# Performance work log

Hardware: AMD Instinct MI355X
Metric: run time of the kernel (lower is better)

The kernel has to match this reference:

```python
import jax, jax.numpy as jnp
import numpy as np

N = 4096
IN_DIM = 512
NUM_HEADS = 8
SUB_DIM = 64
ETA = 0.5
LAMBDA_SPARSE = 0.1
EDGE_PROB = 0.01


def setup_inputs() -> dict:
    key = jax.random.key(0)
    k_h, k_u, k_a = jax.random.split(key, 3)
    H = jax.random.normal(k_h, (N, IN_DIM), dtype=jnp.float32)
    # Per-head orthonormal subspace bases (QR init, as in the torch module)
    raw = jax.random.normal(k_u, (NUM_HEADS, IN_DIM, SUB_DIM), dtype=jnp.float32)
    U = jax.vmap(lambda a: jnp.linalg.qr(a)[0])(raw)  # [K, in_dim, r]
    # Binary adjacency mask with self-loops (float 0/1)
    adj = (jax.random.uniform(k_a, (N, N)) < EDGE_PROB).astype(jnp.float32)
    adj_mask = jnp.maximum(adj, jnp.eye(N, dtype=jnp.float32))
    threshold = jnp.full((IN_DIM,), LAMBDA_SPARSE, dtype=jnp.float32)
    return {"H": H, "adj_mask": adj_mask, "U": U, "threshold": threshold}


def reference(H, adj_mask, U, threshold):
    r = U.shape[-1]
    scale = jnp.asarray(r, H.dtype) ** 0.5
    # Z_k = U_k^T H^T  -> [K, r, n]
    Z = jnp.einsum('kdr,nd->krn', U, H)
    # scores[k, i, j] = Z_k[:, i] . Z_k[:, j] / sqrt(r), masked to neighbors
    scores = jnp.einsum('kri,krj->kij', Z, Z) / scale
    scores = scores + (1.0 - adj_mask) * (-1e9)
    alpha = jax.nn.softmax(scores, axis=-1)          # [K, n, n]
    # Z_agg[k, :, i] = sum_j alpha[k, i, j] * Z_k[:, j]
    Z_agg = jnp.einsum('krj,kij->kri', Z, alpha)      # [K, r, n]
    # project back and sum heads: [n, d]
    agg = jnp.einsum('kdr,kri->id', U, Z_agg)
    H_half = H + ETA * agg
    H_out = jax.nn.relu(H_half - threshold[None, :])
    # orthogonality loss: sum_{k<l} ||U_k^T U_l||_F^2
    gram = jnp.einsum('kdr,lds->klrs', U, U)
    sq = jnp.sum(gram ** 2, axis=(-1, -2))            # [K, K]
    orth_loss = 0.5 * (jnp.sum(sq) - jnp.trace(sq))
    return H_out, orth_loss
```

## Files before the change

kernel.cpp:

```cpp
#include <hip/hip_runtime.h>
#include <hip/hip_bf16.h>

#define NN   4096
#define DD   512
#define KH   8
#define RR   64
#define CAP  128

typedef unsigned short u16;
typedef unsigned int   u32;
typedef __attribute__((ext_vector_type(8))) short short8;
typedef __attribute__((ext_vector_type(4))) float f32x4;

__device__ __forceinline__ float bflo(u32 v){ union{u32 i; float f;} c; c.i = v << 16;        return c.f; }
__device__ __forceinline__ float bfhi(u32 v){ union{u32 i; float f;} c; c.i = v & 0xFFFF0000u; return c.f; }
__device__ __forceinline__ u16 f2bf(float f){ __hip_bfloat16 h = __float2bfloat16(f); return *reinterpret_cast<u16*>(&h); }

__global__ __launch_bounds__(256) void prep_scan(const float* __restrict__ H, const float* __restrict__ U,
                                                 const float* __restrict__ adj,
                                                 u16* __restrict__ Hb, u16* __restrict__ Bt1,
                                                 u16* __restrict__ Bt2,
                                                 int* __restrict__ nlist, int* __restrict__ cnt,
                                                 float* __restrict__ lossP) {
    union SH {
        struct { float tile[64][65]; int list[CAP]; int cntS; } p;
        struct { float UkT[64][20]; float UlT[64][68]; } o;
    };
    __shared__ SH sh;
    __shared__ float red4[4];
    const int b = blockIdx.x, t = threadIdx.x;
    if (b < 4096) {
        const int i = b;
        if (t == 0) sh.p.cntS = 0;
        __syncthreads();
        const float* arow = adj + (size_t)i * NN;
        #pragma unroll
        for (int qq = 0; qq < 4; qq++) {
            int j = (qq * 256 + t) * 4;
            float4 mv = *(const float4*)(arow + j);
            if (mv.x != 0.f) { int p = atomicAdd(&sh.p.cntS, 1); if (p < CAP) sh.p.list[p] = j;     }
            if (mv.y != 0.f) { int p = atomicAdd(&sh.p.cntS, 1); if (p < CAP) sh.p.list[p] = j + 1; }
            if (mv.z != 0.f) { int p = atomicAdd(&sh.p.cntS, 1); if (p < CAP) sh.p.list[p] = j + 2; }
            if (mv.w != 0.f) { int p = atomicAdd(&sh.p.cntS, 1); if (p < CAP) sh.p.list[p] = j + 3; }
        }
        __syncthreads();
        const int n = min(sh.p.cntS, CAP);
        if (t < n) nlist[(size_t)i * CAP + t] = sh.p.list[t];
        if (t == 0) cnt[i] = n;
        return;
    }
    if (b < 6144) {
        size_t id = (size_t)(b - 4096) * 256 + t;
        float4 v = *(const float4*)(H + id * 4);
        ushort4 o; o.x = f2bf(v.x); o.y = f2bf(v.y); o.z = f2bf(v.z); o.w = f2bf(v.w);
        *(ushort4*)(Hb + id * 4) = o;
        return;
    }
    if (b < 6208) {
        const int b2 = b - 6144;
        const int k = b2 >> 3, d0 = (b2 & 7) * 64;
        #pragma unroll
        for (int s = 0; s < 4; s++) {
            int u = t + 256 * s;
            int dd = u >> 4, rq = u & 15;
            float4 v = *(const float4*)(U + ((size_t)(k * DD + d0 + dd)) * RR + rq * 4);
            sh.p.tile[dd][rq * 4 + 0] = v.x; sh.p.tile[dd][rq * 4 + 1] = v.y;
            sh.p.tile[dd][rq * 4 + 2] = v.z; sh.p.tile[dd][rq * 4 + 3] = v.w;
        }
        __syncthreads();
        {   int r = t >> 2;
            #pragma unroll
            for (int ii = 0; ii < 16; ii++) {
                int dd = (t & 3) * 16 + ii;
                Bt1[(size_t)(k * RR + r) * DD + d0 + dd] = f2bf(sh.p.tile[dd][r]);
            }
        }
        {   int dd = t >> 2, rb = (t & 3) * 16;
            #pragma unroll
            for (int ii = 0; ii < 16; ii++) {
                Bt2[(size_t)(d0 + dd) * DD + k * RR + rb + ii] = f2bf(sh.p.tile[dd][rb + ii]);
            }
        }
        return;
    }
    const int ob = b - 6208;
    const int pb = ob >> 2, strip = ob & 3;
    int idx = pb, k = 0, lh = 1;
    #pragma unroll
    for (int kk = 0; kk < 8; kk++) {
        int c = 7 - kk;
        if (idx < c) { k = kk; lh = kk + 1 + idx; break; }
        idx -= c;
    }
    const int r = t & 15;
    const int s0 = (t >> 4) * 4;
    const int r0g = strip * 16;
    const float* Uk = U + (size_t)k  * DD * RR;
    const float* Ul = U + (size_t)lh * DD * RR;
    float a0 = 0.f, a1 = 0.f, a2 = 0.f, a3 = 0.f;
    for (int dc = 0; dc < DD; dc += 64) {
        {   int dd = t >> 2, rq = t & 3;
            *(float4*)&sh.o.UkT[dd][rq * 4] = *(const float4*)(Uk + (size_t)(dc + dd) * RR + r0g + rq * 4);
        }
        #pragma unroll
        for (int s = 0; s < 4; s++) {
            int u = t + 256 * s;
            int dd = u >> 4, sq = u & 15;
            *(float4*)&sh.o.UlT[dd][sq * 4] = *(const float4*)(Ul + (size_t)(dc + dd) * RR + sq * 4);
        }
        __syncthreads();
        #pragma unroll 4
        for (int dd = 0; dd < 64; dd++) {
            float a = sh.o.UkT[dd][r];
            float4 bv = *(const float4*)&sh.o.UlT[dd][s0];
            a0 += a * bv.x; a1 += a * bv.y; a2 += a * bv.z; a3 += a * bv.w;
        }
        __syncthreads();
    }
    float v = a0 * a0 + a1 * a1 + a2 * a2 + a3 * a3;
    #pragma unroll
    for (int off = 32; off; off >>= 1) v += __shfl_down(v, off, 64);
    if ((t & 63) == 0) red4[t >> 6] = v;
    __syncthreads();
    if (t == 0) lossP[ob] = red4[0] + red4[1] + red4[2] + red4[3];
}

__global__ __launch_bounds__(256) void zgemm_mfma(const u16* __restrict__ Hb, const u16* __restrict__ Bt1,
                                                  u16* __restrict__ Zb) {
    __shared__ short As[64][72];
    __shared__ short Bs[64][72];
    const int t = threadIdx.x;
    const int i0 = blockIdx.x * 64, n0 = blockIdx.y * 64;
    const int w = t >> 6, lane = t & 63;
    const int lm = lane & 15, lg = lane >> 4;
    f32x4 acc[4] = {};
    for (int kc = 0; kc < DD; kc += 64) {
        #pragma unroll
        for (int s = 0; s < 2; s++) {
            int c = t + 256 * s; int row = c >> 3, g = c & 7;
            *(short8*)&As[row][g * 8] = *(const short8*)(Hb  + (size_t)(i0 + row) * DD + kc + g * 8);
            *(short8*)&Bs[row][g * 8] = *(const short8*)(Bt1 + (size_t)(n0 + row) * DD + kc + g * 8);
        }
        __syncthreads();
        #pragma unroll
        for (int ks = 0; ks < 64; ks += 32) {
            short8 af = *(const short8*)&As[w * 16 + lm][ks + lg * 8];
            #pragma unroll
            for (int b = 0; b < 4; b++) {
                short8 bfr = *(const short8*)&Bs[b * 16 + lm][ks + lg * 8];
                acc[b] = __builtin_amdgcn_mfma_f32_16x16x32_bf16(af, bfr, acc[b], 0, 0, 0);
            }
        }
        __syncthreads();
    }
    #pragma unroll
    for (int b = 0; b < 4; b++)
        #pragma unroll
        for (int q = 0; q < 4; q++) {
            int row = i0 + w * 16 + lg * 4 + q;
            int col = n0 + b * 16 + lm;
            Zb[(size_t)row * DD + col] = f2bf(acc[b][q]);
        }
}

__global__ __launch_bounds__(512) void attn11(const u16* __restrict__ Zb, const int* __restrict__ nlist,
                                              const int* __restrict__ cnt, u16* __restrict__ Zaggb) {
    const int i = blockIdx.x, t = threadIdx.x;
    const int w = t >> 6, lane = t & 63;
    __shared__ int   nbrS[CAP];
    __shared__ float red[KH][DD];
    __shared__ float lS[KH][KH + 1];
    const int ci = cnt[i];
    if (t < CAP) nbrS[t] = nlist[(size_t)i * CAP + min(t, ci - 1)];
    __syncthreads();

    float a[8];
    {
        uint4 av = *(const uint4*)(Zb + (size_t)i * DD + lane * 8);
        a[0] = bflo(av.x); a[1] = bfhi(av.x); a[2] = bflo(av.y); a[3] = bfhi(av.y);
        a[4] = bflo(av.z); a[5] = bfhi(av.z); a[6] = bflo(av.w); a[7] = bfhi(av.w);
    }

    float l = 0.f;
    float acc[8] = {};
    const int nIt = (ci + 7) >> 3;

    uint4 b0 = *(const uint4*)(Zb + (size_t)nbrS[w] * DD + lane * 8);
    uint4 b1 = *(const uint4*)(Zb + (size_t)nbrS[min(w + 8, CAP - 1)] * DD + lane * 8);

    #define PROCESS(c, val)                                                        \
    {   float zf[8];                                                               \
        zf[0] = bflo(c.x); zf[1] = bfhi(c.x); zf[2] = bflo(c.y); zf[3] = bfhi(c.y);\
        zf[4] = bflo(c.z); zf[5] = bfhi(c.z); zf[6] = bflo(c.w); zf[7] = bfhi(c.w);\
        float s = zf[0]*a[0] + zf[1]*a[1] + zf[2]*a[2] + zf[3]*a[3]                \
                + zf[4]*a[4] + zf[5]*a[5] + zf[6]*a[6] + zf[7]*a[7];               \
        s += __shfl_xor(s, 1); s += __shfl_xor(s, 2); s += __shfl_xor(s, 4);       \
        const float e = (val) ? __expf(s * 0.125f) : 0.f;                          \
        l += e;                                                                    \
        _Pragma("unroll")                                                          \
        for (int d = 0; d < 8; d++) acc[d] += e * zf[d];                           \
    }

    for (int tt = 0; tt < nIt; tt += 2) {
        {
            const uint4 c = b0;
            const int pf = min(w + 8 * (tt + 2), CAP - 1);
            b0 = *(const uint4*)(Zb + (size_t)nbrS[pf] * DD + lane * 8);
            const bool val = (w + 8 * tt) < ci;
            PROCESS(c, val);
        }
        if (tt + 1 < nIt) {
            const uint4 c = b1;
            const int pf = min(w + 8 * (tt + 3), CAP - 1);
            b1 = *(const uint4*)(Zb + (size_t)nbrS[pf] * DD + lane * 8);
            const bool val = (w + 8 * (tt + 1)) < ci;
            PROCESS(c, val);
        }
    }
    #undef PROCESS

    *(float4*)&red[w][lane * 8]     = make_float4(acc[0], acc[1], acc[2], acc[3]);
    *(float4*)&red[w][lane * 8 + 4] = make_float4(acc[4], acc[5], acc[6], acc[7]);
    if ((lane & 7) == 0) lS[w][lane >> 3] = l;
    __syncthreads();

    const int d = t, k = d >> 6;
    float ls = 0.f, sum = 0.f;
    #pragma unroll
    for (int ww = 0; ww < KH; ww++) { ls += lS[ww][k]; sum += red[ww][d]; }
    Zaggb[(size_t)i * DD + d] = f2bf(sum / ls);
}

__global__ __launch_bounds__(256) void outgemm_mfma(const u16* __restrict__ Ab, const u16* __restrict__ Btb,
                                                    const float* __restrict__ H, const float* __restrict__ thr,
                                                    const float* __restrict__ lossP,
                                                    float* __restrict__ out) {
    __shared__ short As[64][72];
    __shared__ short Bs[64][72];
    const int t = threadIdx.x;
    const int i0 = blockIdx.x * 64, n0 = blockIdx.y * 64;
    if (i0 == 0 && n0 == 0 && t < 64) {
        float v = lossP[t] + ((t + 64 < 112) ? lossP[t + 64] : 0.f);
        #pragma unroll
        for (int off = 32; off; off >>= 1) v += __shfl_down(v, off, 64);
        if (t == 0) out[(size_t)NN * DD] = v;
    }
    const int w = t >> 6, lane = t & 63;
    const int lm = lane & 15, lg = lane >> 4;
    f32x4 acc[4] = {};
    for (int kc = 0; kc < DD; kc += 64) {
        #pragma unroll
        for (int s = 0; s < 2; s++) {
            int c = t + 256 * s; int row = c >> 3, g = c & 7;
            *(short8*)&As[row][g * 8] = *(const short8*)(Ab  + (size_t)(i0 + row) * DD + kc + g * 8);
            *(short8*)&Bs[row][g * 8] = *(const short8*)(Btb + (size_t)(n0 + row) * DD + kc + g * 8);
        }
        __syncthreads();
        #pragma unroll
        for (int ks = 0; ks < 64; ks += 32) {
            short8 af = *(const short8*)&As[w * 16 + lm][ks + lg * 8];
            #pragma unroll
            for (int b = 0; b < 4; b++) {
                short8 bfr = *(const short8*)&Bs[b * 16 + lm][ks + lg * 8];
                acc[b] = __builtin_amdgcn_mfma_f32_16x16x32_bf16(af, bfr, acc[b], 0, 0, 0);
            }
        }
        __syncthreads();
    }
    #pragma unroll
    for (int b = 0; b < 4; b++) {
        const int col = n0 + b * 16 + lm;
        const float th = thr[col];
        #pragma unroll
        for (int q = 0; q < 4; q++) {
            int row = i0 + w * 16 + lg * 4 + q;
            float h = H[(size_t)row * DD + col];
            out[(size_t)row * DD + col] = fmaxf(h + 0.5f * acc[b][q] - th, 0.f);
        }
    }
}

extern "C" void kernel_launch(void* const* d_in, const int* in_sizes, int n_in,
                              void* d_out, int out_size, void* d_ws, size_t ws_size,
                              hipStream_t stream) {
    const float* H   = (const float*)d_in[0];
    const float* adj = (const float*)d_in[1];
    const float* U   = (const float*)d_in[2];
    const float* thr = (const float*)d_in[3];
    float* out = (float*)d_out;

    char* ws = (char*)d_ws;
    float* lossP = (float*)ws;
    u16*   Hb    = (u16*)(ws + 1024);
    u16*   Zb    = (u16*)(ws + 1024 + 4u * 1024 * 1024);
    u16*   Zaggb = (u16*)(ws + 1024 + 8u * 1024 * 1024);
    u16*   Bt1   = (u16*)(ws + 1024 + 12u * 1024 * 1024);
    u16*   Bt2   = (u16*)(ws + 1024 + 12u * 1024 * 1024 + 512u * 1024);
    int*   nlist = (int*)(ws + 1024 + 13u * 1024 * 1024);
    int*   cnt   = (int*)(ws + 1024 + 15u * 1024 * 1024 + 512u * 1024);

    prep_scan<<<6320, 256, 0, stream>>>(H, U, adj, Hb, Bt1, Bt2, nlist, cnt, lossP);
    zgemm_mfma<<<dim3(64, 8), 256, 0, stream>>>(Hb, Bt1, Zb);
    attn11<<<NN, 512, 0, stream>>>(Zb, nlist, cnt, Zaggb);
    outgemm_mfma<<<dim3(64, 8), 256, 0, stream>>>(Zaggb, Bt2, H, thr, lossP, out);
}
```

Measured before the change: 173.6 us.

## Use wave-ballot compaction for adjacency scan and reorder prep blocks

The adjacency scan now gives each wavefront one row and compacts neighbor indices with ballot/popcount prefix sums, instead of one block per row using shared-memory atomics. This removes the atomic contention and the block-level syncs, and makes each thread issue 16 independent float4 loads. The slow orthogonality-loss blocks move to the front of the grid and use smaller d-chunks, so that long-latency work starts first. Neighbor order is now deterministic. The larger unrolled load set raises register pressure.

```diff
diff --git a/kernel.cpp b/kernel.cpp
--- a/kernel.cpp
+++ b/kernel.cpp
@@ -9,6 +9,7 @@
 
 typedef unsigned short u16;
 typedef unsigned int   u32;
+typedef unsigned long long u64;
 typedef __attribute__((ext_vector_type(8))) short short8;
 typedef __attribute__((ext_vector_type(4))) float f32x4;
 
@@ -23,106 +24,119 @@
                                                  int* __restrict__ nlist, int* __restrict__ cnt,
                                                  float* __restrict__ lossP) {
     union SH {
-        struct { float tile[64][65]; int list[CAP]; int cntS; } p;
-        struct { float UkT[64][20]; float UlT[64][68]; } o;
+        float tile[64][65];
+        struct { float UkT[32][20]; float UlT[32][68]; } o;
     };
     __shared__ SH sh;
     __shared__ float red4[4];
     const int b = blockIdx.x, t = threadIdx.x;
-    if (b < 4096) {
-        const int i = b;
-        if (t == 0) sh.p.cntS = 0;
-        __syncthreads();
-        const float* arow = adj + (size_t)i * NN;
-        #pragma unroll
-        for (int qq = 0; qq < 4; qq++) {
-            int j = (qq * 256 + t) * 4;
-            float4 mv = *(const float4*)(arow + j);
-            if (mv.x != 0.f) { int p = atomicAdd(&sh.p.cntS, 1); if (p < CAP) sh.p.list[p] = j;     }
-            if (mv.y != 0.f) { int p = atomicAdd(&sh.p.cntS, 1); if (p < CAP) sh.p.list[p] = j + 1; }
-            if (mv.z != 0.f) { int p = atomicAdd(&sh.p.cntS, 1); if (p < CAP) sh.p.list[p] = j + 2; }
-            if (mv.w != 0.f) { int p = atomicAdd(&sh.p.cntS, 1); if (p < CAP) sh.p.list[p] = j + 3; }
-        }
-        __syncthreads();
-        const int n = min(sh.p.cntS, CAP);
-        if (t < n) nlist[(size_t)i * CAP + t] = sh.p.list[t];
-        if (t == 0) cnt[i] = n;
+
+    if (b < 112) {
+        const int ob = b;
+        const int pb = ob >> 2, strip = ob & 3;
+        int idx = pb, k = 0, lh = 1;
+        #pragma unroll
+        for (int kk = 0; kk < 8; kk++) {
+            int c = 7 - kk;
+            if (idx < c) { k = kk; lh = kk + 1 + idx; break; }
+            idx -= c;
+        }
+        const int r = t & 15;
+        const int s0 = (t >> 4) * 4;
+        const int r0g = strip * 16;
+        const float* Uk = U + (size_t)k  * DD * RR;
+        const float* Ul = U + (size_t)lh * DD * RR;
+        float a0 = 0.f, a1 = 0.f, a2 = 0.f, a3 = 0.f;
+        for (int dc = 0; dc < DD; dc += 32) {
+            if (t < 128) {
+                int dd = t >> 2, rq = t & 3;
+                *(float4*)&sh.o.UkT[dd][rq * 4] = *(const float4*)(Uk + (size_t)(dc + dd) * RR + r0g + rq * 4);
+            }
+            #pragma unroll
+            for (int s = 0; s < 2; s++) {
+                int u = t + 256 * s;
+                int dd = u >> 4, sq = u & 15;
+                *(float4*)&sh.o.UlT[dd][sq * 4] = *(const float4*)(Ul + (size_t)(dc + dd) * RR + sq * 4);
+            }
+            __syncthreads();
+            #pragma unroll 4
+            for (int dd = 0; dd < 32; dd++) {
+                float a = sh.o.UkT[dd][r];
+                float4 bv = *(const float4*)&sh.o.UlT[dd][s0];
+                a0 += a * bv.x; a1 += a * bv.y; a2 += a * bv.z; a3 += a * bv.w;
+            }
+            __syncthreads();
+        }
+        float v = a0 * a0 + a1 * a1 + a2 * a2 + a3 * a3;
+        #pragma unroll
+        for (int off = 32; off; off >>= 1) v += __shfl_down(v, off, 64);
+        if ((t & 63) == 0) red4[t >> 6] = v;
+        __syncthreads();
+        if (t == 0) lossP[ob] = red4[0] + red4[1] + red4[2] + red4[3];
         return;
     }
-    if (b < 6144) {
-        size_t id = (size_t)(b - 4096) * 256 + t;
-        float4 v = *(const float4*)(H + id * 4);
-        ushort4 o; o.x = f2bf(v.x); o.y = f2bf(v.y); o.z = f2bf(v.z); o.w = f2bf(v.w);
-        *(ushort4*)(Hb + id * 4) = o;
-        return;
-    }
-    if (b < 6208) {
-        const int b2 = b - 6144;
+    if (b < 176) {
+        const int b2 = b - 112;
         const int k = b2 >> 3, d0 = (b2 & 7) * 64;
         #pragma unroll
         for (int s = 0; s < 4; s++) {
             int u = t + 256 * s;
             int dd = u >> 4, rq = u & 15;
             float4 v = *(const float4*)(U + ((size_t)(k * DD + d0 + dd)) * RR + rq * 4);
-            sh.p.tile[dd][rq * 4 + 0] = v.x; sh.p.tile[dd][rq * 4 + 1] = v.y;
-            sh.p.tile[dd][rq * 4 + 2] = v.z; sh.p.tile[dd][rq * 4 + 3] = v.w;
+            sh.tile[dd][rq * 4 + 0] = v.x; sh.tile[dd][rq * 4 + 1] = v.y;
+            sh.tile[dd][rq * 4 + 2] = v.z; sh.tile[dd][rq * 4 + 3] = v.w;
         }
         __syncthreads();
         {   int r = t >> 2;
             #pragma unroll
             for (int ii = 0; ii < 16; ii++) {
                 int dd = (t & 3) * 16 + ii;
-                Bt1[(size_t)(k * RR + r) * DD + d0 + dd] = f2bf(sh.p.tile[dd][r]);
+                Bt1[(size_t)(k * RR + r) * DD + d0 + dd] = f2bf(sh.tile[dd][r]);
             }
         }
         {   int dd = t >> 2, rb = (t & 3) * 16;
             #pragma unroll
             for (int ii = 0; ii < 16; ii++) {
-                Bt2[(size_t)(d0 + dd) * DD + k * RR + rb + ii] = f2bf(sh.p.tile[dd][rb + ii]);
+                Bt2[(size_t)(d0 + dd) * DD + k * RR + rb + ii] = f2bf(sh.tile[dd][rb + ii]);
             }
         }
         return;
     }
-    const int ob = b - 6208;
-    const int pb = ob >> 2, strip = ob & 3;
-    int idx = pb, k = 0, lh = 1;
-    #pragma unroll
-    for (int kk = 0; kk < 8; kk++) {
-        int c = 7 - kk;
-        if (idx < c) { k = kk; lh = kk + 1 + idx; break; }
-        idx -= c;
-    }
-    const int r = t & 15;
-    const int s0 = (t >> 4) * 4;
-    const int r0g = strip * 16;
-    const float* Uk = U + (size_t)k  * DD * RR;
-    const float* Ul = U + (size_t)lh * DD * RR;
-    float a0 = 0.f, a1 = 0.f, a2 = 0.f, a3 = 0.f;
-    for (int dc = 0; dc < DD; dc += 64) {
-        {   int dd = t >> 2, rq = t & 3;
-            *(float4*)&sh.o.UkT[dd][rq * 4] = *(const float4*)(Uk + (size_t)(dc + dd) * RR + r0g + rq * 4);
-        }
-        #pragma unroll
-        for (int s = 0; s < 4; s++) {
-            int u = t + 256 * s;
-            int dd = u >> 4, sq = u & 15;
-            *(float4*)&sh.o.UlT[dd][sq * 4] = *(const float4*)(Ul + (size_t)(dc + dd) * RR + sq * 4);
-        }
-        __syncthreads();
-        #pragma unroll 4
-        for (int dd = 0; dd < 64; dd++) {
-            float a = sh.o.UkT[dd][r];
-            float4 bv = *(const float4*)&sh.o.UlT[dd][s0];
-            a0 += a * bv.x; a1 += a * bv.y; a2 += a * bv.z; a3 += a * bv.w;
-        }
-        __syncthreads();
-    }
-    float v = a0 * a0 + a1 * a1 + a2 * a2 + a3 * a3;
-    #pragma unroll
-    for (int off = 32; off; off >>= 1) v += __shfl_down(v, off, 64);
-    if ((t & 63) == 0) red4[t >> 6] = v;
-    __syncthreads();
-    if (t == 0) lossP[ob] = red4[0] + red4[1] + red4[2] + red4[3];
+    if (b < 1200) {
+        const int row = (b - 176) * 4 + (t >> 6);
+        const int lane = t & 63;
+        const float* arow = adj + (size_t)row * NN;
+        int* ndst = nlist + (size_t)row * CAP;
+        const u64 lt = (1ull << lane) - 1;
+        int base = 0;
+        #pragma unroll
+        for (int h = 0; h < 2; h++) {
+            float4 mv[8];
+            #pragma unroll
+            for (int c = 0; c < 8; c++)
+                mv[c] = *(const float4*)(arow + (h * 8 + c) * 256 + lane * 4);
+            #pragma unroll
+            for (int c = 0; c < 8; c++) {
+                const int j = (h * 8 + c) * 256 + lane * 4;
+                const u64 bx = __ballot(mv[c].x != 0.f);
+                const u64 by = __ballot(mv[c].y != 0.f);
+                const u64 bz = __ballot(mv[c].z != 0.f);
+                const u64 bw = __ballot(mv[c].w != 0.f);
+                const int nx = __popcll(bx), ny = __popcll(by), nz = __popcll(bz);
+                if (mv[c].x != 0.f) { int p = base + __popcll(bx & lt);                if (p < CAP) ndst[p] = j;     }
+                if (mv[c].y != 0.f) { int p = base + nx + __popcll(by & lt);           if (p < CAP) ndst[p] = j + 1; }
+                if (mv[c].z != 0.f) { int p = base + nx + ny + __popcll(bz & lt);      if (p < CAP) ndst[p] = j + 2; }
+                if (mv[c].w != 0.f) { int p = base + nx + ny + nz + __popcll(bw & lt); if (p < CAP) ndst[p] = j + 3; }
+                base += nx + ny + nz + __popcll(bw);
+            }
+        }
+        if (lane == 0) cnt[row] = min(base, CAP);
+        return;
+    }
+    size_t id = (size_t)(b - 1200) * 256 + t;
+    float4 v = *(const float4*)(H + id * 4);
+    ushort4 o; o.x = f2bf(v.x); o.y = f2bf(v.y); o.z = f2bf(v.z); o.w = f2bf(v.w);
+    *(ushort4*)(Hb + id * 4) = o;
 }
 
 __global__ __launch_bounds__(256) void zgemm_mfma(const u16* __restrict__ Hb, const u16* __restrict__ Bt1,
@@ -202,8 +216,7 @@
     }
 
     for (int tt = 0; tt < nIt; tt += 2) {
-        {
-            const uint4 c = b0;
+        {   const uint4 c = b0;
             const int pf = min(w + 8 * (tt + 2), CAP - 1);
             b0 = *(const uint4*)(Zb + (size_t)nbrS[pf] * DD + lane * 8);
             const bool val = (w + 8 * tt) < ci;
@@ -299,7 +312,7 @@
     int*   nlist = (int*)(ws + 1024 + 13u * 1024 * 1024);
     int*   cnt   = (int*)(ws + 1024 + 15u * 1024 * 1024 + 512u * 1024);
 
-    prep_scan<<<6320, 256, 0, stream>>>(H, U, adj, Hb, Bt1, Bt2, nlist, cnt, lossP);
+    prep_scan<<<3248, 256, 0, stream>>>(H, U, adj, Hb, Bt1, Bt2, nlist, cnt, lossP);
     zgemm_mfma<<<dim3(64, 8), 256, 0, stream>>>(Hb, Bt1, Zb);
     attn11<<<NN, 512, 0, stream>>>(Zb, nlist, cnt, Zaggb);
     outgemm_mfma<<<dim3(64, 8), 256, 0, stream>>>(Zaggb, Bt2, H, thr, lossP, out);
```

Result: faster. 157.1 us (-9.5%).
